# Optimization experiments

Measured on AMD Instinct MI355X. Metric: run time of the kernel, lower is better.

## Reference

```python
import jax, jax.numpy as jnp
import numpy as np

BIG = 1e9  # finite stand-in for float('inf') border padding (grad-safe)


def setup_inputs() -> dict:
    key = jax.random.key(0)
    k1, k2 = jax.random.split(key)
    B, L1, L2, F = 32, 1024, 1024, 128
    return {
        "seq1": jax.random.normal(k1, (B, L1, F), dtype=jnp.float32),
        "seq2": jax.random.normal(k2, (B, L2, F), dtype=jnp.float32),
        "scale_weights": jnp.ones((1,), dtype=jnp.float32),  # nn.Parameter ones(num_scales)/num_scales -> softmax-normalized anyway
    }


def _dtw_similarity(seq1, seq2):
    """Vectorized (anti-diagonal wavefront) version of MultiScaleDTW._compute_dtw.

    Same recurrence: D[i,j] = ||s1[i-1]-s2[j-1]|| + min(D[i-1,j-1], D[i-1,j], D[i,j-1]),
    D[0,0]=0, first row/col = inf. Returns similarity = 1/(1 + D[L1,L2]/(L1+L2)).
    """
    B, L1, F = seq1.shape
    L2 = seq2.shape[1]
    # pairwise L2 distance matrix (B, L1, L2) via |a|^2 + |b|^2 - 2 a.b (one GEMM)
    sq1 = jnp.sum(seq1 * seq1, axis=-1)
    sq2 = jnp.sum(seq2 * seq2, axis=-1)
    dot = jnp.einsum('bif,bjf->bij', seq1, seq2)
    C = jnp.sqrt(jnp.maximum(sq1[:, :, None] + sq2[:, None, :] - 2.0 * dot, 0.0))

    i_idx = jnp.arange(L1 + 1)
    # diagonal k holds D[i, k-i] for i in [0, L1]
    d0 = jnp.full((B, L1 + 1), BIG, jnp.float32).at[:, 0].set(0.0)  # k=0: D[0,0]=0
    d1 = jnp.full((B, L1 + 1), BIG, jnp.float32)                     # k=1: borders = inf

    def shift(x):  # x[:, i] -> x[:, i-1], pad with BIG
        return jnp.concatenate([jnp.full((B, 1), BIG, x.dtype), x[:, :-1]], axis=1)

    def step(carry, k):
        prev2, prev = carry  # diagonals k-2, k-1
        j = k - i_idx
        row = jnp.clip(i_idx - 1, 0, L1 - 1)
        col = jnp.clip(j - 1, 0, L2 - 1)
        c = C[:, row, col]  # (B, L1+1) cost along the diagonal
        m = jnp.minimum(shift(prev2), jnp.minimum(shift(prev), prev))
        cur = c + m
        valid = (i_idx >= 1) & (i_idx <= L1) & (j >= 1) & (j <= L2)
        cur = jnp.where(valid[None, :], cur, BIG)
        return (prev, cur), None

    (_, last), _ = jax.lax.scan(step, (d0, d1), jnp.arange(2, L1 + L2 + 1))
    dtw_dist = last[:, L1] / (L1 + L2)  # D[L1, L2] / (L1 + L2)
    return 1.0 / (1.0 + dtw_dist)


def reference(seq1, seq2, scale_weights):
    # num_scales = 1: softmax over single scale weight -> 1.0; only scale-0 DTW runs
    w = jax.nn.softmax(scale_weights, axis=0)
    sim = _dtw_similarity(seq1, seq2)
    return w[0] * sim  # combined_similarity, shape (B,)
```

## Files before the change

### kernel.cpp

```cpp
#include <hip/hip_runtime.h>
#include <hip/hip_bf16.h>

#define BIGV 1.0e9f

static constexpr int B_ = 32;
static constexpr int L_ = 1024;
static constexpr int F_ = 128;
static constexpr int UD2_ = 592;
static constexpr int LAGP_ = 96;
static constexpr int NSEGP_ = 42;
static constexpr size_t STREAM_US = (size_t)B_ * 2 * UD2_ * 1024;

typedef __attribute__((ext_vector_type(8))) short short8;
typedef __attribute__((ext_vector_type(4))) float f32x4;

__device__ __forceinline__ unsigned pack2(float x, float y) {
  unsigned r;
  asm("v_cvt_pk_bf16_f32 %0, %1, %2" : "=v"(r) : "v"(x), "v"(y));
  return r;
}

__device__ __forceinline__ float shfl_up1_dpp(float x) {
  int xi = __float_as_int(x);
  int r = __builtin_amdgcn_update_dpp(xi, xi, 0x138, 0xF, 0xF, false);
  return __int_as_float(r);
}

__device__ __forceinline__ float dpp_odd(float x) {
  int xi = __float_as_int(x);
  int r = __builtin_amdgcn_update_dpp(xi, xi, 0xF5, 0xF, 0xF, false);
  return __int_as_float(r);
}

__device__ __forceinline__ float min3f(float a, float b, float c) {
  float r;
  asm("v_min3_f32 %0, %1, %2, %3" : "=v"(r) : "v"(a), "v"(b), "v"(c));
  return r;
}

__device__ __forceinline__ float fsqrt(float x) {
  float r;
  asm("v_sqrt_f32 %0, %1" : "=v"(r) : "v"(x));
  return r;
}

__global__ void norm_kernel(const float* __restrict__ s1, const float* __restrict__ s2,
                            float* __restrict__ nrm) {
  int gt   = blockIdx.x * blockDim.x + threadIdx.x;
  int wid  = gt >> 6;
  int lane = gt & 63;
  const float* src = (wid < B_ * L_) ? (s1 + (size_t)wid * F_)
                                     : (s2 + (size_t)(wid - B_ * L_) * F_);
  float2 v = ((const float2*)src)[lane];
  float s = v.x * v.x + v.y * v.y;
#pragma unroll
  for (int o = 32; o > 0; o >>= 1) s += __shfl_xor(s, o, 64);
  if (lane == 0) nrm[wid] = s;
}

__global__ __launch_bounds__(512) void cost_kernel(const float* __restrict__ s1,
                                                   const float* __restrict__ s2,
                                                   ushort* __restrict__ stream,
                                                   const float* __restrict__ nrm) {
  __shared__ __align__(16) ushort sbuf[2 * 128 * 136];
  __shared__ float q1[128], q2[128];
  short (*aL)[136] = (short(*)[136])sbuf;
  short (*bL)[136] = (short(*)[136])(sbuf + 128 * 136);
  ushort (*stage)[256] = (ushort(*)[256])sbuf;

  const int tid = threadIdx.x;
  const int b   = blockIdx.y;
  const int tc  = blockIdx.x & 7;
  const int tr  = blockIdx.x >> 3;

  const float* Ap = s1 + (size_t)b * L_ * F_ + (size_t)tr * 128 * F_;
  const float* Bp = s2 + (size_t)b * L_ * F_ + (size_t)tc * 128 * F_;

#pragma unroll 4
  for (int it = 0; it < 8; ++it) {
    int idx = it * 2048 + tid * 4;
    int r = idx >> 7, cc = idx & 127;
    float4 va = *(const float4*)(Ap + idx);
    float4 vb = *(const float4*)(Bp + idx);
    *(uint2*)&aL[r][cc] = make_uint2(pack2(va.x, va.y), pack2(va.z, va.w));
    *(uint2*)&bL[r][cc] = make_uint2(pack2(vb.x, vb.y), pack2(vb.z, vb.w));
  }
  if (tid < 128) q1[tid] = nrm[(size_t)b * L_ + tr * 128 + tid];
  else if (tid < 256) q2[tid - 128] = nrm[(size_t)B_ * L_ + (size_t)b * L_ + tc * 128 + (tid - 128)];
  __syncthreads();

  const int wave = tid >> 6, lane = tid & 63, quad = lane >> 4, l16 = lane & 15;
  const int m0 = (wave & 3) * 32, n0 = (wave >> 2) * 64;

  f32x4 acc[2][4] = {};
#pragma unroll
  for (int kc = 0; kc < 4; ++kc) {
    short8 af[2], bf[4];
#pragma unroll
    for (int mi = 0; mi < 2; ++mi)
      af[mi] = *(const short8*)&aL[m0 + mi * 16 + l16][kc * 32 + quad * 8];
#pragma unroll
    for (int nj = 0; nj < 4; ++nj)
      bf[nj] = *(const short8*)&bL[n0 + nj * 16 + l16][kc * 32 + quad * 8];
#pragma unroll
    for (int mi = 0; mi < 2; ++mi)
#pragma unroll
      for (int nj = 0; nj < 4; ++nj)
        acc[mi][nj] = __builtin_amdgcn_mfma_f32_16x16x32_bf16(af[mi], bf[nj], acc[mi][nj], 0, 0, 0);
  }

  __syncthreads();

#pragma unroll
  for (int mi = 0; mi < 2; ++mi) {
    int lr0 = m0 + mi * 16 + quad * 4;
    float a0 = q1[lr0 + 0], a1 = q1[lr0 + 1], a2 = q1[lr0 + 2], a3 = q1[lr0 + 3];
#pragma unroll
    for (int nj = 0; nj < 4; ++nj) {
      int lc = n0 + nj * 16 + l16;
      float qc = q2[lc];
      float v0 = fsqrt(fmaxf(a0 + qc - 2.0f * acc[mi][nj][0], 0.0f));
      float v1 = fsqrt(fmaxf(a1 + qc - 2.0f * acc[mi][nj][1], 0.0f));
      float v2 = fsqrt(fmaxf(a2 + qc - 2.0f * acc[mi][nj][2], 0.0f));
      float v3 = fsqrt(fmaxf(a3 + qc - 2.0f * acc[mi][nj][3], 0.0f));
      float o0 = dpp_odd(v0), o1 = dpp_odd(v1), o2 = dpp_odd(v2), o3 = dpp_odd(v3);
      if ((l16 & 1) == 0) {
        int u = (lr0 >> 3) + (lc >> 1);
        uint4 wd = make_uint4(pack2(v0, o0), pack2(v1, o1), pack2(v2, o2), pack2(v3, o3));
        *(uint4*)&stage[u][lr0 * 2] = wd;
      }
    }
  }
  __syncthreads();

  const int w        = tr >> 2;
  const int slotbase = 256 * (tr & 3);
  const int ubase    = tc * 64 + 16 * (tr & 3);
  ushort* Sb = stream + ((size_t)(b * 2 + w) * UD2_ + ubase) * 1024 + slotbase;
#pragma unroll
  for (int it = 0; it < 5; ++it) {
    int t = it * 512 + tid;
    if (t < 80 * 32) {
      int u = t >> 5, h = t & 31, g = h >> 1;
      if ((unsigned)(u - g) < 64u)
        *(uint4*)(Sb + (size_t)u * 1024 + g * 16 + (h & 1) * 8) =
            *(const uint4*)&stage[u][g * 16 + (h & 1) * 8];
    }
  }
}

#define PAIR_STEP(C0HEAD, C1HEAD)                                   \
  {                                                                 \
    unsigned wds[8] = {cwA.x, cwA.y, cwA.z, cwA.w,                  \
                       cwB.x, cwB.y, cwB.z, cwB.w};                 \
    float cv0[8], cv1[8];                                           \
    _Pragma("unroll") for (int r = 0; r < 8; ++r) {                 \
      cv0[r] = __uint_as_float(wds[r] << 16);                       \
      cv1[r] = __uint_as_float(wds[r] & 0xFFFF0000u);               \
    }                                                               \
    float nlA[8], nlB[8];                                           \
    float curA = (C0HEAD) + min3f(dg0, up0, left[0]);               \
    nlA[0] = curA;                                                  \
    _Pragma("unroll") for (int r = 1; r < 8; ++r) {                 \
      curA = cv0[r] + min3f(left[r - 1], left[r], curA);            \
      nlA[r] = curA;                                                \
    }                                                               \
    float curB = (C1HEAD) + min3f(up0, up1, nlA[0]);                \
    nlB[0] = curB;                                                  \
    _Pragma("unroll") for (int r = 1; r < 8; ++r) {                 \
      curB = cv1[r] + min3f(nlA[r - 1], nlA[r], curB);              \
      nlB[r] = curB;                                                \
    }                                                               \
    _Pragma("unroll") for (int r = 0; r < 8; ++r) left[r] = nlB[r]; \
    bot0 = nlA[7]; bot1 = nlB[7];                                   \
  }

__global__ __launch_bounds__(128, 1) void dtw_kernel(const ushort* __restrict__ stream,
                                                     float* __restrict__ out) {
  __shared__ float hand[1040];

  const int b    = blockIdx.x;
  const int tid  = threadIdx.x;
  const int wave = tid >> 6;
  const int lane = tid & 63;
  const bool l0 = (lane == 0);

  const ushort* src = stream + (size_t)(b * 2 + wave) * UD2_ * 1024 + lane * 16;

  float left[8];
#pragma unroll
  for (int r = 0; r < 8; ++r) left[r] = BIGV;
  float bot0 = BIGV, bot1 = BIGV;
  float shAprev = BIGV, hPv = BIGV, result = 0.0f;
  float2 hR[4];
  float hb0[16], hb1[16];
  uint4 pre0[16], pre1[16];

#pragma unroll
  for (int i = 0; i < 16; ++i) {
    pre0[i] = *(const uint4*)(src + (size_t)i * 1024);
    pre1[i] = *(const uint4*)(src + (size_t)i * 1024 + 8);
  }

  for (int n = 0; n < NSEGP_; ++n) {
    __syncthreads();
    const int tBase = 16 * n - (wave ? LAGP_ : 0);
    if ((unsigned)tBase >= 576u) continue;

    const bool fast = (tBase >= 64) & (tBase <= 496);

    if (wave == 0) {
      if (fast) {
#pragma unroll
        for (int k = 0; k < 16; ++k) {
          float shA = shfl_up1_dpp(bot1);
          float shB = shfl_up1_dpp(bot0);
          uint4 cwA = pre0[k], cwB = pre1[k];
          const ushort* p = src + (size_t)(tBase + k + 16) * 1024;
          pre0[k] = *(const uint4*)p;
          pre1[k] = *(const uint4*)(p + 8);
          float dg0 = l0 ? BIGV : shAprev;
          float up0 = l0 ? BIGV : shB;
          float up1 = l0 ? BIGV : shA;
          PAIR_STEP(cv0[0], cv1[0])
          shAprev = shA;
          hb0[k] = bot0; hb1[k] = bot1;
        }
        if (lane == 63) {
          float2* hp = (float2*)&hand[2 * tBase - 126];
#pragma unroll
          for (int q = 0; q < 16; ++q) hp[q] = make_float2(hb0[q], hb1[q]);
        }
      } else {
#pragma unroll
        for (int k = 0; k < 16; ++k) {
          const int t = tBase + k;
          float shA = shfl_up1_dpp(bot1);
          float shB = shfl_up1_dpp(bot0);
          uint4 cwA = pre0[k], cwB = pre1[k];
          const ushort* p = src + (size_t)(tBase + k + 16) * 1024;
          pre0[k] = *(const uint4*)p;
          pre1[k] = *(const uint4*)(p + 8);
          float dg0 = l0 ? ((t == 0) ? 0.0f : BIGV) : shAprev;
          float up0 = l0 ? BIGV : shB;
          float up1 = l0 ? BIGV : shA;
          bool act = ((unsigned)(t - lane) < 512u);
          PAIR_STEP(act ? cv0[0] : BIGV, act ? cv1[0] : BIGV)
          shAprev = shA;
          int j = 2 * t - 126;
          if (lane == 63 && (unsigned)j < 1024u) {
            hand[j] = bot0; hand[j + 1] = bot1;
          }
        }
      }
    } else {
      if (fast) {
#pragma unroll
        for (int i = 0; i < 4; ++i) hR[i] = *(const float2*)&hand[2 * (tBase + i)];
#pragma unroll
        for (int k = 0; k < 16; ++k) {
          float shA = shfl_up1_dpp(bot1);
          float shB = shfl_up1_dpp(bot0);
          float2 hCur = hR[k & 3];
          uint4 cwA = pre0[k], cwB = pre1[k];
          const ushort* p = src + (size_t)(tBase + k + 16) * 1024;
          pre0[k] = *(const uint4*)p;
          pre1[k] = *(const uint4*)(p + 8);
          hR[k & 3] = *(const float2*)&hand[2 * (tBase + k + 4)];
          float dg0 = l0 ? hPv : shAprev;
          float up0 = l0 ? hCur.x : shB;
          float up1 = l0 ? hCur.y : shA;
          PAIR_STEP(cv0[0], cv1[0])
          shAprev = shA;
          hPv = hCur.y;
        }
      } else {
#pragma unroll
        for (int i = 0; i < 4; ++i)
          hR[i] = *(const float2*)&hand[(2 * (tBase + i)) & 1023];
#pragma unroll
        for (int k = 0; k < 16; ++k) {
          const int t = tBase + k;
          float shA = shfl_up1_dpp(bot1);
          float shB = shfl_up1_dpp(bot0);
          float2 hCur = hR[k & 3];
          uint4 cwA = pre0[k], cwB = pre1[k];
          const ushort* p = src + (size_t)(tBase + k + 16) * 1024;
          pre0[k] = *(const uint4*)p;
          pre1[k] = *(const uint4*)(p + 8);
          hR[k & 3] = *(const float2*)&hand[(2 * (t + 4)) & 1023];
          float dg0 = l0 ? hPv : shAprev;
          float up0 = l0 ? hCur.x : shB;
          float up1 = l0 ? hCur.y : shA;
          bool act = ((unsigned)(t - lane) < 512u);
          PAIR_STEP(act ? cv0[0] : BIGV, act ? cv1[0] : BIGV)
          shAprev = shA;
          hPv = hCur.y;
          if (t == 574) result = bot1;
        }
      }
    }
  }
  if (wave == 1 && lane == 63) out[b] = 1.0f / (1.0f + result * (1.0f / 2048.0f));
}

extern "C" void kernel_launch(void* const* d_in, const int* in_sizes, int n_in,
                              void* d_out, int out_size, void* d_ws, size_t ws_size,
                              hipStream_t stream_) {
  const float* s1 = (const float*)d_in[0];
  const float* s2 = (const float*)d_in[1];
  float* out = (float*)d_out;
  ushort* cws = (ushort*)d_ws;
  float* nrm = (float*)(cws + STREAM_US);

  norm_kernel<<<dim3((2 * B_ * L_) / 4), 256, 0, stream_>>>(s1, s2, nrm);
  cost_kernel<<<dim3(64, B_), 512, 0, stream_>>>(s1, s2, cws, nrm);
  dtw_kernel<<<dim3(B_), 128, 0, stream_>>>(cws, out);
}
```

Baseline: 212.5 us.

## Fuse norm, cost and DTW into one kernel with per-tile readiness flags

Merges the three launches into a single persistent-style kernel. The first 32 blocks run the DTW wavefront and the rest produce cost tiles, publishing completion through per-batch atomic bitmask flags. DTW waves spin-wait on the flags for just the tiles they need, so the wavefront overlaps with cost generation. Row norms are now computed inside the cost blocks with LDS atomics, which removes the separate norm pass. The risks are that correctness depends on the DTW blocks being co-resident with the producer blocks (there is a guard-limited spin), the LDS atomic adds are extra work, and a memset launch is added.

Result: slower. 400.8 us (+88.6%).

```diff
diff --git a/kernel.cpp b/kernel.cpp
--- a/kernel.cpp
+++ b/kernel.cpp
@@ -44,109 +44,15 @@
   return r;
 }
 
-__global__ void norm_kernel(const float* __restrict__ s1, const float* __restrict__ s2,
-                            float* __restrict__ nrm) {
-  int gt   = blockIdx.x * blockDim.x + threadIdx.x;
-  int wid  = gt >> 6;
-  int lane = gt & 63;
-  const float* src = (wid < B_ * L_) ? (s1 + (size_t)wid * F_)
-                                     : (s2 + (size_t)(wid - B_ * L_) * F_);
-  float2 v = ((const float2*)src)[lane];
-  float s = v.x * v.x + v.y * v.y;
-#pragma unroll
-  for (int o = 32; o > 0; o >>= 1) s += __shfl_xor(s, o, 64);
-  if (lane == 0) nrm[wid] = s;
-}
-
-__global__ __launch_bounds__(512) void cost_kernel(const float* __restrict__ s1,
-                                                   const float* __restrict__ s2,
-                                                   ushort* __restrict__ stream,
-                                                   const float* __restrict__ nrm) {
-  __shared__ __align__(16) ushort sbuf[2 * 128 * 136];
-  __shared__ float q1[128], q2[128];
-  short (*aL)[136] = (short(*)[136])sbuf;
-  short (*bL)[136] = (short(*)[136])(sbuf + 128 * 136);
-  ushort (*stage)[256] = (ushort(*)[256])sbuf;
-
-  const int tid = threadIdx.x;
-  const int b   = blockIdx.y;
-  const int tc  = blockIdx.x & 7;
-  const int tr  = blockIdx.x >> 3;
-
-  const float* Ap = s1 + (size_t)b * L_ * F_ + (size_t)tr * 128 * F_;
-  const float* Bp = s2 + (size_t)b * L_ * F_ + (size_t)tc * 128 * F_;
-
-#pragma unroll 4
-  for (int it = 0; it < 8; ++it) {
-    int idx = it * 2048 + tid * 4;
-    int r = idx >> 7, cc = idx & 127;
-    float4 va = *(const float4*)(Ap + idx);
-    float4 vb = *(const float4*)(Bp + idx);
-    *(uint2*)&aL[r][cc] = make_uint2(pack2(va.x, va.y), pack2(va.z, va.w));
-    *(uint2*)&bL[r][cc] = make_uint2(pack2(vb.x, vb.y), pack2(vb.z, vb.w));
-  }
-  if (tid < 128) q1[tid] = nrm[(size_t)b * L_ + tr * 128 + tid];
-  else if (tid < 256) q2[tid - 128] = nrm[(size_t)B_ * L_ + (size_t)b * L_ + tc * 128 + (tid - 128)];
-  __syncthreads();
-
-  const int wave = tid >> 6, lane = tid & 63, quad = lane >> 4, l16 = lane & 15;
-  const int m0 = (wave & 3) * 32, n0 = (wave >> 2) * 64;
-
-  f32x4 acc[2][4] = {};
-#pragma unroll
-  for (int kc = 0; kc < 4; ++kc) {
-    short8 af[2], bf[4];
-#pragma unroll
-    for (int mi = 0; mi < 2; ++mi)
-      af[mi] = *(const short8*)&aL[m0 + mi * 16 + l16][kc * 32 + quad * 8];
-#pragma unroll
-    for (int nj = 0; nj < 4; ++nj)
-      bf[nj] = *(const short8*)&bL[n0 + nj * 16 + l16][kc * 32 + quad * 8];
-#pragma unroll
-    for (int mi = 0; mi < 2; ++mi)
-#pragma unroll
-      for (int nj = 0; nj < 4; ++nj)
-        acc[mi][nj] = __builtin_amdgcn_mfma_f32_16x16x32_bf16(af[mi], bf[nj], acc[mi][nj], 0, 0, 0);
-  }
-
-  __syncthreads();
-
-#pragma unroll
-  for (int mi = 0; mi < 2; ++mi) {
-    int lr0 = m0 + mi * 16 + quad * 4;
-    float a0 = q1[lr0 + 0], a1 = q1[lr0 + 1], a2 = q1[lr0 + 2], a3 = q1[lr0 + 3];
-#pragma unroll
-    for (int nj = 0; nj < 4; ++nj) {
-      int lc = n0 + nj * 16 + l16;
-      float qc = q2[lc];
-      float v0 = fsqrt(fmaxf(a0 + qc - 2.0f * acc[mi][nj][0], 0.0f));
-      float v1 = fsqrt(fmaxf(a1 + qc - 2.0f * acc[mi][nj][1], 0.0f));
-      float v2 = fsqrt(fmaxf(a2 + qc - 2.0f * acc[mi][nj][2], 0.0f));
-      float v3 = fsqrt(fmaxf(a3 + qc - 2.0f * acc[mi][nj][3], 0.0f));
-      float o0 = dpp_odd(v0), o1 = dpp_odd(v1), o2 = dpp_odd(v2), o3 = dpp_odd(v3);
-      if ((l16 & 1) == 0) {
-        int u = (lr0 >> 3) + (lc >> 1);
-        uint4 wd = make_uint4(pack2(v0, o0), pack2(v1, o1), pack2(v2, o2), pack2(v3, o3));
-        *(uint4*)&stage[u][lr0 * 2] = wd;
-      }
-    }
-  }
-  __syncthreads();
-
-  const int w        = tr >> 2;
-  const int slotbase = 256 * (tr & 3);
-  const int ubase    = tc * 64 + 16 * (tr & 3);
-  ushort* Sb = stream + ((size_t)(b * 2 + w) * UD2_ + ubase) * 1024 + slotbase;
-#pragma unroll
-  for (int it = 0; it < 5; ++it) {
-    int t = it * 512 + tid;
-    if (t < 80 * 32) {
-      int u = t >> 5, h = t & 31, g = h >> 1;
-      if ((unsigned)(u - g) < 64u)
-        *(uint4*)(Sb + (size_t)u * 1024 + g * 16 + (h & 1) * 8) =
-            *(const uint4*)&stage[u][g * 16 + (h & 1) * 8];
-    }
-  }
+__device__ __forceinline__ void wait_tiles(unsigned* flag, unsigned need, bool l0) {
+  if (l0) {
+    int guard = 0;
+    while ((atomicOr(flag, 0u) & need) != need) {
+      __builtin_amdgcn_s_sleep(8);
+      if (++guard > 1000000) break;
+    }
+  }
+  __threadfence();
 }
 
 #define PAIR_STEP(C0HEAD, C1HEAD)                                   \
@@ -175,15 +81,126 @@
     bot0 = nlA[7]; bot1 = nlB[7];                                   \
   }
 
-__global__ __launch_bounds__(128, 1) void dtw_kernel(const ushort* __restrict__ stream,
-                                                     float* __restrict__ out) {
-  __shared__ float hand[1040];
-
-  const int b    = blockIdx.x;
-  const int tid  = threadIdx.x;
+__global__ __launch_bounds__(512, 1) void fused_kernel(const float* __restrict__ s1,
+                                                       const float* __restrict__ s2,
+                                                       ushort* __restrict__ stream,
+                                                       unsigned* __restrict__ flags,
+                                                       float* __restrict__ out) {
+  __shared__ __align__(16) ushort sbuf[2 * 128 * 136];
+  __shared__ float q1[128], q2[128];
+
+  const int bid = blockIdx.x;
+  const int tid = threadIdx.x;
+
+  if (bid >= 32) {
+    const int c     = bid - 32;
+    const int p     = c >> 6;
+    const int batch = (c >> 1) & 31;
+    const int w     = c & 1;
+    const int tc    = p >> 2;
+    const int j     = p & 3;
+    const int tr    = w * 4 + j;
+
+    short (*aL)[136] = (short(*)[136])sbuf;
+    short (*bL)[136] = (short(*)[136])(sbuf + 128 * 136);
+    ushort (*stage)[256] = (ushort(*)[256])sbuf;
+
+    const float* Ap = s1 + (size_t)batch * L_ * F_ + (size_t)tr * 128 * F_;
+    const float* Bp = s2 + (size_t)batch * L_ * F_ + (size_t)tc * 128 * F_;
+
+    if (tid < 128) q1[tid] = 0.0f;
+    else if (tid < 256) q2[tid - 128] = 0.0f;
+    __syncthreads();
+
+#pragma unroll 4
+    for (int it = 0; it < 8; ++it) {
+      int idx = it * 2048 + tid * 4;
+      int r = idx >> 7, cc = idx & 127;
+      float4 va = *(const float4*)(Ap + idx);
+      float4 vb = *(const float4*)(Bp + idx);
+      *(uint2*)&aL[r][cc] = make_uint2(pack2(va.x, va.y), pack2(va.z, va.w));
+      *(uint2*)&bL[r][cc] = make_uint2(pack2(vb.x, vb.y), pack2(vb.z, vb.w));
+      atomicAdd(&q1[r], va.x * va.x + va.y * va.y + va.z * va.z + va.w * va.w);
+      atomicAdd(&q2[r], vb.x * vb.x + vb.y * vb.y + vb.z * vb.z + vb.w * vb.w);
+    }
+    __syncthreads();
+
+    const int wave = tid >> 6, lane = tid & 63, quad = lane >> 4, l16 = lane & 15;
+    const int m0 = (wave & 3) * 32, n0 = (wave >> 2) * 64;
+
+    f32x4 acc[2][4] = {};
+#pragma unroll
+    for (int kc = 0; kc < 4; ++kc) {
+      short8 af[2], bf[4];
+#pragma unroll
+      for (int mi = 0; mi < 2; ++mi)
+        af[mi] = *(const short8*)&aL[m0 + mi * 16 + l16][kc * 32 + quad * 8];
+#pragma unroll
+      for (int nj = 0; nj < 4; ++nj)
+        bf[nj] = *(const short8*)&bL[n0 + nj * 16 + l16][kc * 32 + quad * 8];
+#pragma unroll
+      for (int mi = 0; mi < 2; ++mi)
+#pragma unroll
+        for (int nj = 0; nj < 4; ++nj)
+          acc[mi][nj] = __builtin_amdgcn_mfma_f32_16x16x32_bf16(af[mi], bf[nj], acc[mi][nj], 0, 0, 0);
+    }
+
+    __syncthreads();
+
+#pragma unroll
+    for (int mi = 0; mi < 2; ++mi) {
+      int lr0 = m0 + mi * 16 + quad * 4;
+      float a0 = q1[lr0 + 0], a1 = q1[lr0 + 1], a2 = q1[lr0 + 2], a3 = q1[lr0 + 3];
+#pragma unroll
+      for (int nj = 0; nj < 4; ++nj) {
+        int lc = n0 + nj * 16 + l16;
+        float qc = q2[lc];
+        float v0 = fsqrt(fmaxf(a0 + qc - 2.0f * acc[mi][nj][0], 0.0f));
+        float v1 = fsqrt(fmaxf(a1 + qc - 2.0f * acc[mi][nj][1], 0.0f));
+        float v2 = fsqrt(fmaxf(a2 + qc - 2.0f * acc[mi][nj][2], 0.0f));
+        float v3 = fsqrt(fmaxf(a3 + qc - 2.0f * acc[mi][nj][3], 0.0f));
+        float o0 = dpp_odd(v0), o1 = dpp_odd(v1), o2 = dpp_odd(v2), o3 = dpp_odd(v3);
+        if ((l16 & 1) == 0) {
+          int u = (lr0 >> 3) + (lc >> 1);
+          uint4 wd = make_uint4(pack2(v0, o0), pack2(v1, o1), pack2(v2, o2), pack2(v3, o3));
+          *(uint4*)&stage[u][lr0 * 2] = wd;
+        }
+      }
+    }
+    __syncthreads();
+
+    const int slotbase = 256 * j;
+    ushort* Sb = stream + ((size_t)(batch * 2 + w) * UD2_ + 16 * p) * 1024 + slotbase;
+#pragma unroll
+    for (int it = 0; it < 5; ++it) {
+      int t = it * 512 + tid;
+      if (t < 80 * 32) {
+        int u = t >> 5, h = t & 31, g = h >> 1;
+        if ((unsigned)(u - g) < 64u)
+          *(uint4*)(Sb + (size_t)u * 1024 + g * 16 + (h & 1) * 8) =
+              *(const uint4*)&stage[u][g * 16 + (h & 1) * 8];
+      }
+    }
+    __syncthreads();
+    if (tid == 0) {
+      __threadfence();
+      atomicOr(&flags[batch * 2 + w], 1u << p);
+    }
+    return;
+  }
+
+  if (tid >= 128) {
+    for (int n = 0; n < NSEGP_; ++n) __syncthreads();
+    return;
+  }
+
+  float* hand = (float*)sbuf;
+
+  const int b    = bid;
   const int wave = tid >> 6;
   const int lane = tid & 63;
   const bool l0 = (lane == 0);
+  unsigned* flagS = &flags[b * 2 + wave];
 
   const ushort* src = stream + (size_t)(b * 2 + wave) * UD2_ * 1024 + lane * 16;
 
@@ -196,6 +213,7 @@
   float hb0[16], hb1[16];
   uint4 pre0[16], pre1[16];
 
+  wait_tiles(flagS, 1u, l0);
 #pragma unroll
   for (int i = 0; i < 16; ++i) {
     pre0[i] = *(const uint4*)(src + (size_t)i * 1024);
@@ -206,6 +224,13 @@
     __syncthreads();
     const int tBase = 16 * n - (wave ? LAGP_ : 0);
     if ((unsigned)tBase >= 576u) continue;
+
+    {
+      unsigned P = (unsigned)(tBase + 31) >> 4;
+      if (P > 31u) P = 31u;
+      unsigned need = (P >= 31u) ? 0xFFFFFFFFu : ((1u << (P + 1)) - 1u);
+      wait_tiles(flagS, need, l0);
+    }
 
     const bool fast = (tBase >= 64) & (tBase <= 496);
 
@@ -247,9 +272,9 @@
           bool act = ((unsigned)(t - lane) < 512u);
           PAIR_STEP(act ? cv0[0] : BIGV, act ? cv1[0] : BIGV)
           shAprev = shA;
-          int j = 2 * t - 126;
-          if (lane == 63 && (unsigned)j < 1024u) {
-            hand[j] = bot0; hand[j + 1] = bot1;
+          int jj = 2 * t - 126;
+          if (lane == 63 && (unsigned)jj < 1024u) {
+            hand[jj] = bot0; hand[jj + 1] = bot1;
           }
         }
       }
@@ -311,9 +336,8 @@
   const float* s2 = (const float*)d_in[1];
   float* out = (float*)d_out;
   ushort* cws = (ushort*)d_ws;
-  float* nrm = (float*)(cws + STREAM_US);
-
-  norm_kernel<<<dim3((2 * B_ * L_) / 4), 256, 0, stream_>>>(s1, s2, nrm);
-  cost_kernel<<<dim3(64, B_), 512, 0, stream_>>>(s1, s2, cws, nrm);
-  dtw_kernel<<<dim3(B_), 128, 0, stream_>>>(cws, out);
-}
+  unsigned* flags = (unsigned*)(cws + STREAM_US);
+
+  hipMemsetAsync(flags, 0, 64 * sizeof(unsigned), stream_);
+  fused_kernel<<<dim3(32 + 2048), 512, 0, stream_>>>(s1, s2, cws, flags, out);
+}
```
